# Optimization experiments

Hardware: AMD Instinct MI355X
Metric: run time of the kernel (lower is better)

The kernel has to match this reference:

```python
import jax, jax.numpy as jnp
import numpy as np

DIM = 4096  # hadamard_dim, power of 2 -> K=1, pure FWHT with 1/sqrt(n) scaling


def fwht(x):
    """Fast Walsh-Hadamard transform along the last axis, normalized by 1/sqrt(n).

    Butterfly network: log2(n) stages of pairwise add/sub. Matches the math of
    multiplying by the normalized n x n Hadamard matrix (x @ H / sqrt(n)).
    """
    orig_shape = x.shape
    n = orig_shape[-1]
    x = x.reshape(-1, n)
    h = 1
    while h < n:  # static unrolled loop over log2(n) stages (n is static)
        # view as [rows, n/(2h), 2, h]; butterfly pairs are (s=0, s=1)
        xb = x.reshape(-1, n // (2 * h), 2, h)
        a = xb[:, :, 0, :]
        b = xb[:, :, 1, :]
        x = jnp.stack([a + b, a - b], axis=2).reshape(-1, n)
        h *= 2
    scale = jnp.asarray(1.0 / np.sqrt(n), dtype=x.dtype)
    return (x * scale).reshape(orig_shape)


def setup_inputs() -> dict:
    key = jax.random.key(0)
    x = jax.random.normal(key, (4, 2048, DIM), dtype=jnp.float32)
    return {"x": x}


def reference(x):
    # force_fp32=True path: compute in fp32 (x already fp32), cast back to input dtype
    x_dtype = x.dtype
    y = fwht(x.astype(jnp.float32))
    return y.astype(x_dtype)
```

## Files before the change

### kernel.cpp

```cpp
#include <hip/hip_runtime.h>


using v4 = __attribute__((ext_vector_type(4))) float;

__device__ __forceinline__ void had16(float x[16]) {
#pragma unroll
    for (int h = 1; h < 16; h <<= 1) {
#pragma unroll
        for (int i = 0; i < 16; ++i) {
            if (!(i & h)) {
                float a = x[i], b = x[i ^ h];
                x[i] = a + b; x[i ^ h] = a - b;
            }
        }
    }
}

__global__ void __launch_bounds__(256) fwht4096_kernel(const float* __restrict__ in,
                                                       float* __restrict__ out) {
    __shared__ float lds[4096];
    const int t = threadIdx.x;
    const size_t base = (size_t)blockIdx.x * 4096;
    const v4* in4 = reinterpret_cast<const v4*>(in + base);
    v4* out4 = reinterpret_cast<v4*>(out + base);

    v4 v[4];
#pragma unroll
    for (int j = 0; j < 4; ++j) v[j] = __builtin_nontemporal_load(&in4[t + 256 * j]);

#pragma unroll
    for (int j = 0; j < 4; ++j) {
        float a = v[j][0], b = v[j][1], c = v[j][2], d = v[j][3];
        float ab = a + b, amb = a - b, cd = c + d, cmd = c - d;
        v[j][0] = ab + cd; v[j][1] = amb + cmd; v[j][2] = ab - cd; v[j][3] = amb - cmd;
    }
    {
        v4 s0 = v[0] + v[1], d0 = v[0] - v[1];
        v4 s1 = v[2] + v[3], d1 = v[2] - v[3];
        v[0] = s0 + s1; v[2] = s0 - s1;
        v[1] = d0 + d1; v[3] = d0 - d1;
    }
    {
        v4* l4 = reinterpret_cast<v4*>(lds);
        const int wb = t ^ ((t >> 4) & 7);
#pragma unroll
        for (int j = 0; j < 4; ++j) l4[wb + 256 * j] = v[j];
    }
    __syncthreads();

    float x[16];

    {
        const int b2 = (t & 3) + 64 * (t >> 2);
        const int s2 = (t >> 2) & 7;
#pragma unroll
        for (int r = 0; r < 16; ++r) x[r] = lds[b2 + 4 * (r ^ s2)];
        had16(x);
#pragma unroll
        for (int r = 0; r < 16; ++r) lds[b2 + 4 * (r ^ s2)] = x[r];
    }
    __syncthreads();

    {
        const int l = t & 63, w = t >> 6;
        const int b3 = 1024 * w;
#pragma unroll
        for (int r = 0; r < 16; ++r) x[r] = lds[(l ^ ((r & 7) << 2)) + 64 * r + b3];
        had16(x);
        const float scale = 0.015625f;
#pragma unroll
        for (int r = 0; r < 16; ++r) lds[(l ^ ((r & 7) << 2)) + 64 * r + b3] = x[r] * scale;
    }
    __syncthreads();

    {
        const v4* l4 = reinterpret_cast<const v4*>(lds);
        const int wb = t ^ ((t >> 4) & 7);
#pragma unroll
        for (int j = 0; j < 4; ++j) {
            v4 o = l4[wb + 256 * j];
            __builtin_nontemporal_store(o, &out4[t + 256 * j]);
        }
    }
}

extern "C" void kernel_launch(void* const* d_in, const int* in_sizes, int n_in,
                              void* d_out, int out_size, void* d_ws, size_t ws_size,
                              hipStream_t stream) {
    const float* x = (const float*)d_in[0];
    float* out = (float*)d_out;
    const int rows = in_sizes[0] >> 12;
    fwht4096_kernel<<<dim3(rows), dim3(256), 0, stream>>>(x, out);
}
```

Measured before the change: 217.3 us.

## Load input directly into LDS and reorder FWHT stages around swizzled layout

```diff
diff --git a/kernel.cpp b/kernel.cpp
--- a/kernel.cpp
+++ b/kernel.cpp
@@ -20,65 +20,63 @@
                                                        float* __restrict__ out) {
     __shared__ float lds[4096];
     const int t = threadIdx.x;
+    const int l = t & 63, w = t >> 6;
     const size_t base = (size_t)blockIdx.x * 4096;
-    const v4* in4 = reinterpret_cast<const v4*>(in + base);
-    v4* out4 = reinterpret_cast<v4*>(out + base);
-
-    v4 v[4];
-#pragma unroll
-    for (int j = 0; j < 4; ++j) v[j] = __builtin_nontemporal_load(&in4[t + 256 * j]);
 
 #pragma unroll
     for (int j = 0; j < 4; ++j) {
-        float a = v[j][0], b = v[j][1], c = v[j][2], d = v[j][3];
-        float ab = a + b, amb = a - b, cd = c + d, cmd = c - d;
-        v[j][0] = ab + cd; v[j][1] = amb + cmd; v[j][2] = ab - cd; v[j][3] = amb - cmd;
-    }
-    {
-        v4 s0 = v[0] + v[1], d0 = v[0] - v[1];
-        v4 s1 = v[2] + v[3], d1 = v[2] - v[3];
-        v[0] = s0 + s1; v[2] = s0 - s1;
-        v[1] = d0 + d1; v[3] = d0 - d1;
-    }
-    {
-        v4* l4 = reinterpret_cast<v4*>(lds);
-        const int wb = t ^ ((t >> 4) & 7);
-#pragma unroll
-        for (int j = 0; j < 4; ++j) l4[wb + 256 * j] = v[j];
+        const int K = j | ((w & 1) << 2);
+        const float* gp = in + base + 4 * ((l ^ K) + 64 * j + 256 * w);
+        float* lp = lds + 4 * l + 256 * j + 1024 * w;
+        __builtin_amdgcn_global_load_lds(
+            (const __attribute__((address_space(1))) void*)gp,
+            (__attribute__((address_space(3))) void*)lp, 16, 0, 0);
     }
     __syncthreads();
 
     float x[16];
 
     {
-        const int b2 = (t & 3) + 64 * (t >> 2);
-        const int s2 = (t >> 2) & 7;
+        const int b1 = 1024 * w;
+        const int wx = (w & 1) << 4;
 #pragma unroll
-        for (int r = 0; r < 16; ++r) x[r] = lds[b2 + 4 * (r ^ s2)];
+        for (int r = 0; r < 16; ++r)
+            x[r] = lds[(l ^ ((r >> 2) << 2) ^ wx) + 64 * r + b1];
         had16(x);
 #pragma unroll
-        for (int r = 0; r < 16; ++r) lds[b2 + 4 * (r ^ s2)] = x[r];
+        for (int r = 0; r < 16; ++r)
+            lds[(l ^ ((r >> 2) << 2) ^ wx) + 64 * r + b1] = x[r];
     }
     __syncthreads();
 
     {
-        const int l = t & 63, w = t >> 6;
-        const int b3 = 1024 * w;
+        const int s2 = (t >> 2) & 7;
+        const int base2 = (t & 3) | (((t >> 5) & 3) << 6) | (s2 << 8) | ((t >> 7) << 11);
 #pragma unroll
-        for (int r = 0; r < 16; ++r) x[r] = lds[(l ^ ((r & 7) << 2)) + 64 * r + b3];
+        for (int r = 0; r < 16; ++r) x[r] = lds[base2 + 4 * (r ^ s2)];
         had16(x);
-        const float scale = 0.015625f;
 #pragma unroll
-        for (int r = 0; r < 16; ++r) lds[(l ^ ((r & 7) << 2)) + 64 * r + b3] = x[r] * scale;
+        for (int r = 0; r < 16; ++r) lds[base2 + 4 * (r ^ s2)] = x[r];
     }
     __syncthreads();
 
     {
         const v4* l4 = reinterpret_cast<const v4*>(lds);
-        const int wb = t ^ ((t >> 4) & 7);
+        v4* out4 = reinterpret_cast<v4*>(out + base);
+        const int k3 = (t >> 6) & 3;
 #pragma unroll
         for (int j = 0; j < 4; ++j) {
-            v4 o = l4[wb + 256 * j];
+            v4 vv = l4[(t ^ k3 ^ ((j & 1) << 2)) + 256 * j];
+#pragma unroll
+            for (int e = 0; e < 4; ++e) x[e + 4 * j] = vv[e];
+        }
+        had16(x);
+        const float scale = 0.015625f;
+#pragma unroll
+        for (int j = 0; j < 4; ++j) {
+            v4 o;
+#pragma unroll
+            for (int e = 0; e < 4; ++e) o[e] = x[e + 4 * j] * scale;
             __builtin_nontemporal_store(o, &out4[t + 256 * j]);
         }
     }
```

Result: slower. 229.1 us (+5.4%).

## Process four rows per block with register prefetch of the next row

Applied to the files above, without the earlier changes.

```diff
diff --git a/kernel.cpp b/kernel.cpp
--- a/kernel.cpp
+++ b/kernel.cpp
@@ -16,71 +16,95 @@
     }
 }
 
+#define ROWS_PER_BLOCK 4
+
 __global__ void __launch_bounds__(256) fwht4096_kernel(const float* __restrict__ in,
                                                        float* __restrict__ out) {
     __shared__ float lds[4096];
     const int t = threadIdx.x;
-    const size_t base = (size_t)blockIdx.x * 4096;
-    const v4* in4 = reinterpret_cast<const v4*>(in + base);
-    v4* out4 = reinterpret_cast<v4*>(out + base);
+    const size_t row0 = (size_t)blockIdx.x * ROWS_PER_BLOCK;
 
-    v4 v[4];
+    v4 cur[4];
+    {
+        const v4* in4 = reinterpret_cast<const v4*>(in + row0 * 4096);
 #pragma unroll
-    for (int j = 0; j < 4; ++j) v[j] = __builtin_nontemporal_load(&in4[t + 256 * j]);
+        for (int j = 0; j < 4; ++j) cur[j] = __builtin_nontemporal_load(&in4[t + 256 * j]);
+    }
 
 #pragma unroll
-    for (int j = 0; j < 4; ++j) {
-        float a = v[j][0], b = v[j][1], c = v[j][2], d = v[j][3];
-        float ab = a + b, amb = a - b, cd = c + d, cmd = c - d;
-        v[j][0] = ab + cd; v[j][1] = amb + cmd; v[j][2] = ab - cd; v[j][3] = amb - cmd;
-    }
-    {
-        v4 s0 = v[0] + v[1], d0 = v[0] - v[1];
-        v4 s1 = v[2] + v[3], d1 = v[2] - v[3];
-        v[0] = s0 + s1; v[2] = s0 - s1;
-        v[1] = d0 + d1; v[3] = d0 - d1;
-    }
-    {
-        v4* l4 = reinterpret_cast<v4*>(lds);
-        const int wb = t ^ ((t >> 4) & 7);
-#pragma unroll
-        for (int j = 0; j < 4; ++j) l4[wb + 256 * j] = v[j];
-    }
-    __syncthreads();
+    for (int r = 0; r < ROWS_PER_BLOCK; ++r) {
+        const size_t base = (row0 + r) * 4096;
 
-    float x[16];
-
-    {
-        const int b2 = (t & 3) + 64 * (t >> 2);
-        const int s2 = (t >> 2) & 7;
-#pragma unroll
-        for (int r = 0; r < 16; ++r) x[r] = lds[b2 + 4 * (r ^ s2)];
-        had16(x);
-#pragma unroll
-        for (int r = 0; r < 16; ++r) lds[b2 + 4 * (r ^ s2)] = x[r];
-    }
-    __syncthreads();
-
-    {
-        const int l = t & 63, w = t >> 6;
-        const int b3 = 1024 * w;
-#pragma unroll
-        for (int r = 0; r < 16; ++r) x[r] = lds[(l ^ ((r & 7) << 2)) + 64 * r + b3];
-        had16(x);
-        const float scale = 0.015625f;
-#pragma unroll
-        for (int r = 0; r < 16; ++r) lds[(l ^ ((r & 7) << 2)) + 64 * r + b3] = x[r] * scale;
-    }
-    __syncthreads();
-
-    {
-        const v4* l4 = reinterpret_cast<const v4*>(lds);
-        const int wb = t ^ ((t >> 4) & 7);
 #pragma unroll
         for (int j = 0; j < 4; ++j) {
-            v4 o = l4[wb + 256 * j];
-            __builtin_nontemporal_store(o, &out4[t + 256 * j]);
+            float a = cur[j][0], b = cur[j][1], c = cur[j][2], d = cur[j][3];
+            float ab = a + b, amb = a - b, cd = c + d, cmd = c - d;
+            cur[j][0] = ab + cd; cur[j][1] = amb + cmd;
+            cur[j][2] = ab - cd; cur[j][3] = amb - cmd;
         }
+        {
+            v4 s0 = cur[0] + cur[1], d0 = cur[0] - cur[1];
+            v4 s1 = cur[2] + cur[3], d1 = cur[2] - cur[3];
+            cur[0] = s0 + s1; cur[2] = s0 - s1;
+            cur[1] = d0 + d1; cur[3] = d0 - d1;
+        }
+
+        if (r > 0) __syncthreads();
+
+        {
+            v4* l4 = reinterpret_cast<v4*>(lds);
+            const int wb = t ^ ((t >> 4) & 7);
+#pragma unroll
+            for (int j = 0; j < 4; ++j) l4[wb + 256 * j] = cur[j];
+        }
+
+        v4 nxt[4];
+        if (r + 1 < ROWS_PER_BLOCK) {
+            const v4* in4n = reinterpret_cast<const v4*>(in + (row0 + r + 1) * 4096);
+#pragma unroll
+            for (int j = 0; j < 4; ++j) nxt[j] = __builtin_nontemporal_load(&in4n[t + 256 * j]);
+        }
+        __syncthreads();
+
+        float x[16];
+
+        {
+            const int b2 = (t & 3) + 64 * (t >> 2);
+            const int s2 = (t >> 2) & 7;
+#pragma unroll
+            for (int q = 0; q < 16; ++q) x[q] = lds[b2 + 4 * (q ^ s2)];
+            had16(x);
+#pragma unroll
+            for (int q = 0; q < 16; ++q) lds[b2 + 4 * (q ^ s2)] = x[q];
+        }
+        __syncthreads();
+
+        {
+            const int l = t & 63, w = t >> 6;
+            const int b3 = 1024 * w;
+#pragma unroll
+            for (int q = 0; q < 16; ++q) x[q] = lds[(l ^ ((q & 7) << 2)) + 64 * q + b3];
+            had16(x);
+            const float scale = 0.015625f;
+#pragma unroll
+            for (int q = 0; q < 16; ++q)
+                lds[(l ^ ((q & 7) << 2)) + 64 * q + b3] = x[q] * scale;
+        }
+        __syncthreads();
+
+        {
+            const v4* l4 = reinterpret_cast<const v4*>(lds);
+            v4* out4 = reinterpret_cast<v4*>(out + base);
+            const int wb = t ^ ((t >> 4) & 7);
+#pragma unroll
+            for (int j = 0; j < 4; ++j) {
+                v4 o = l4[wb + 256 * j];
+                __builtin_nontemporal_store(o, &out4[t + 256 * j]);
+            }
+        }
+
+#pragma unroll
+        for (int j = 0; j < 4; ++j) cur[j] = nxt[j];
     }
 }
 
@@ -90,5 +114,5 @@
     const float* x = (const float*)d_in[0];
     float* out = (float*)d_out;
     const int rows = in_sizes[0] >> 12;
-    fwht4096_kernel<<<dim3(rows), dim3(256), 0, stream>>>(x, out);
+    fwht4096_kernel<<<dim3(rows / ROWS_PER_BLOCK), dim3(256), 0, stream>>>(x, out);
 }
```

Result: no change. 221.6 us (+2.0%).

## Process each 4096-row with a single wavefront holding 64 floats per lane

Applied to the files above, without the earlier changes.

```diff
diff --git a/kernel.cpp b/kernel.cpp
--- a/kernel.cpp
+++ b/kernel.cpp
@@ -3,83 +3,73 @@
 
 using v4 = __attribute__((ext_vector_type(4))) float;
 
-__device__ __forceinline__ void had16(float x[16]) {
+__device__ __forceinline__ void had16v(v4 x[16]) {
 #pragma unroll
     for (int h = 1; h < 16; h <<= 1) {
 #pragma unroll
         for (int i = 0; i < 16; ++i) {
             if (!(i & h)) {
-                float a = x[i], b = x[i ^ h];
+                v4 a = x[i], b = x[i ^ h];
                 x[i] = a + b; x[i ^ h] = a - b;
             }
         }
     }
 }
 
-__global__ void __launch_bounds__(256) fwht4096_kernel(const float* __restrict__ in,
-                                                       float* __restrict__ out) {
-    __shared__ float lds[4096];
-    const int t = threadIdx.x;
-    const size_t base = (size_t)blockIdx.x * 4096;
-    const v4* in4 = reinterpret_cast<const v4*>(in + base);
-    v4* out4 = reinterpret_cast<v4*>(out + base);
+__global__ void __launch_bounds__(64) fwht4096_kernel(const float* __restrict__ in,
+                                                      float* __restrict__ out) {
+    __shared__ v4 lds[1024];
+    const int l = threadIdx.x;
+    const size_t base = (size_t)blockIdx.x * 1024;
+    const v4* in4 = reinterpret_cast<const v4*>(in) + base;
+    v4* out4 = reinterpret_cast<v4*>(out) + base;
 
-    v4 v[4];
+    v4 r[16];
 #pragma unroll
-    for (int j = 0; j < 4; ++j) v[j] = __builtin_nontemporal_load(&in4[t + 256 * j]);
+    for (int j = 0; j < 16; ++j) r[j] = __builtin_nontemporal_load(&in4[l + 64 * j]);
 
 #pragma unroll
-    for (int j = 0; j < 4; ++j) {
-        float a = v[j][0], b = v[j][1], c = v[j][2], d = v[j][3];
+    for (int jl = 0; jl < 4; ++jl) {
+        v4 s0 = r[jl] + r[jl + 4], d0 = r[jl] - r[jl + 4];
+        v4 s1 = r[jl + 8] + r[jl + 12], d1 = r[jl + 8] - r[jl + 12];
+        r[jl] = s0 + s1; r[jl + 8] = s0 - s1;
+        r[jl + 4] = d0 + d1; r[jl + 12] = d0 - d1;
+    }
+#pragma unroll
+    for (int j = 0; j < 16; ++j) {
+        float a = r[j][0], b = r[j][1], c = r[j][2], d = r[j][3];
         float ab = a + b, amb = a - b, cd = c + d, cmd = c - d;
-        v[j][0] = ab + cd; v[j][1] = amb + cmd; v[j][2] = ab - cd; v[j][3] = amb - cmd;
+        r[j][0] = ab + cd; r[j][1] = amb + cmd;
+        r[j][2] = ab - cd; r[j][3] = amb - cmd;
     }
     {
-        v4 s0 = v[0] + v[1], d0 = v[0] - v[1];
-        v4 s1 = v[2] + v[3], d1 = v[2] - v[3];
-        v[0] = s0 + s1; v[2] = s0 - s1;
-        v[1] = d0 + d1; v[3] = d0 - d1;
-    }
-    {
-        v4* l4 = reinterpret_cast<v4*>(lds);
-        const int wb = t ^ ((t >> 4) & 7);
+        const int sA = (l >> 4) & 3;
 #pragma unroll
-        for (int j = 0; j < 4; ++j) l4[wb + 256 * j] = v[j];
-    }
-    __syncthreads();
-
-    float x[16];
-
-    {
-        const int b2 = (t & 3) + 64 * (t >> 2);
-        const int s2 = (t >> 2) & 7;
-#pragma unroll
-        for (int r = 0; r < 16; ++r) x[r] = lds[b2 + 4 * (r ^ s2)];
-        had16(x);
-#pragma unroll
-        for (int r = 0; r < 16; ++r) lds[b2 + 4 * (r ^ s2)] = x[r];
+        for (int j = 0; j < 16; ++j)
+            lds[(l + 64 * j) ^ sA ^ ((j & 3) << 2)] = r[j];
     }
     __syncthreads();
 
     {
-        const int l = t & 63, w = t >> 6;
-        const int b3 = 1024 * w;
+        const int sB = l & 15;
 #pragma unroll
-        for (int r = 0; r < 16; ++r) x[r] = lds[(l ^ ((r & 7) << 2)) + 64 * r + b3];
-        had16(x);
-        const float scale = 0.015625f;
+        for (int k = 0; k < 16; ++k) r[k] = lds[16 * l + (k ^ sB)];
+        had16v(r);
 #pragma unroll
-        for (int r = 0; r < 16; ++r) lds[(l ^ ((r & 7) << 2)) + 64 * r + b3] = x[r] * scale;
+        for (int k = 0; k < 16; ++k) lds[16 * l + (k ^ sB)] = r[k];
     }
     __syncthreads();
 
     {
-        const v4* l4 = reinterpret_cast<const v4*>(lds);
-        const int wb = t ^ ((t >> 4) & 7);
+        const int lo = l & 15, hi = (l >> 4) << 8;
 #pragma unroll
-        for (int j = 0; j < 4; ++j) {
-            v4 o = l4[wb + 256 * j];
-            __builtin_nontemporal_store(o, &out4[t + 256 * j]);
+        for (int q = 0; q < 16; ++q) r[q] = lds[(lo ^ q) | (q << 4) | hi];
+        had16v(r);
+        const float scale = 0.015625f;
+#pragma unroll
+        for (int q = 0; q < 16; ++q) {
+            v4 o = r[q] * scale;
+            __builtin_nontemporal_store(o, &out4[lo | (q << 4) | hi]);
         }
     }
 }
@@ -90,5 +80,5 @@
     const float* x = (const float*)d_in[0];
     float* out = (float*)d_out;
     const int rows = in_sizes[0] >> 12;
-    fwht4096_kernel<<<dim3(rows), dim3(256), 0, stream>>>(x, out);
+    fwht4096_kernel<<<dim3(rows), dim3(64), 0, stream>>>(x, out);
 }
```

Result: no change. 219.2 us (+0.9%).
